# Kernel tuning notes

Measured on AMD Instinct MI355X. Metric: run time of the kernel, lower is better.

The kernel has to match this reference:

```python
import jax, jax.numpy as jnp
import numpy as np

N_NODES = 50000
N_EDGES = 800000
D_IN = 256
D_OUT = 256


def setup_inputs() -> dict:
    key = jax.random.key(0)
    ks = jax.random.split(key, 8)
    x = jax.random.normal(ks[0], (N_NODES, D_IN), dtype=jnp.float32)
    edge_index = jax.random.randint(ks[1], (2, N_EDGES), 0, N_NODES, dtype=jnp.int64)
    W_src = jax.random.normal(ks[2], (D_IN, D_OUT), dtype=jnp.float32) * 0.05
    b_src = jax.random.normal(ks[3], (D_OUT,), dtype=jnp.float32) * 0.05
    W_dst = jax.random.normal(ks[4], (D_IN, D_OUT), dtype=jnp.float32) * 0.05
    b_dst = jax.random.normal(ks[5], (D_OUT,), dtype=jnp.float32) * 0.05
    W_self = jax.random.normal(ks[6], (D_IN, D_OUT), dtype=jnp.float32) * 0.05
    b_self = jax.random.normal(ks[7], (D_OUT,), dtype=jnp.float32) * 0.05
    return {"x": x, "edge_index": edge_index, "W_src": W_src, "b_src": b_src,
            "W_dst": W_dst, "b_dst": b_dst, "W_self": W_self, "b_self": b_self}


def reference(x, edge_index, W_src, b_src, W_dst, b_dst, W_self, b_self):
    # LEConv: messages = src_linear(x[row]) - dst_linear(x[col]);
    # scatter-add messages into destination nodes (col); add self_linear(x).
    # Linear commutes with row-gather, so project once on [N, d] then gather.
    row, col = edge_index[0], edge_index[1]
    src = x @ W_src + b_src            # [N, D_OUT]
    dst = x @ W_dst + b_dst            # [N, D_OUT]
    messages = src[row] - dst[col]     # [E, D_OUT]
    agg = jax.ops.segment_sum(messages, col, num_segments=x.shape[0])  # [N, D_OUT]
    return x @ W_self + b_self + agg
```

## Files before the change

### kernel.cpp

```cpp
#include <hip/hip_runtime.h>

#define D 256

typedef unsigned short ushort_t;
typedef unsigned int uint_t;
typedef __attribute__((ext_vector_type(8))) short short8;
typedef __attribute__((ext_vector_type(4))) float floatx4;

static __device__ __forceinline__ ushort_t f2bf(float f) {
    union { float f; uint_t u; } c; c.f = f;
    uint_t r = (c.u + 0x7FFFu + ((c.u >> 16) & 1u)) >> 16;
    return (ushort_t)r;
}
static __device__ __forceinline__ float bf2f(ushort_t b) {
    union { uint_t u; float f; } c; c.u = ((uint_t)b) << 16;
    return c.f;
}

static __device__ __forceinline__ void async16(const void* g, void* l) {
    __builtin_amdgcn_global_load_lds(
        (const __attribute__((address_space(1))) void*)g,
        (__attribute__((address_space(3))) void*)l, 16, 0, 0);
}

__global__ void prep_kernel(const int* __restrict__ col, int* __restrict__ deg,
                            int* __restrict__ rank,
                            const float* __restrict__ x, ushort_t* __restrict__ xh,
                            const float* __restrict__ Wself, const float* __restrict__ Wsrc,
                            const float* __restrict__ Wdst, ushort_t* __restrict__ BT,
                            int E, int total8, int degB, int cvtB) {
    int b = blockIdx.x;
    if (b < degB) {
        int e = b * 256 + threadIdx.x;
        if (e < E) rank[e] = atomicAdd(&deg[col[e]], 1);
    } else if (b < degB + cvtB) {
        int i = (b - degB) * 256 + threadIdx.x;
        if (i >= total8) return;
        float4 a = ((const float4*)x)[i * 2];
        float4 bb = ((const float4*)x)[i * 2 + 1];
        uint4 o;
        o.x = f2bf(a.x) | ((uint_t)f2bf(a.y) << 16);
        o.y = f2bf(a.z) | ((uint_t)f2bf(a.w) << 16);
        o.z = f2bf(bb.x) | ((uint_t)f2bf(bb.y) << 16);
        o.w = f2bf(bb.z) | ((uint_t)f2bf(bb.w) << 16);
        ((uint4*)xh)[i] = o;
    } else {
        int id = (b - degB - cvtB) * 256 + threadIdx.x;
        if (id >= 256 * 768) return;
        int j = id / 768, k = id % 768;
        float v;
        if (k < 256)      v = Wself[(size_t)k * 256 + j];
        else if (k < 512) v = Wsrc [(size_t)(k - 256) * 256 + j];
        else              v = Wdst [(size_t)(k - 512) * 256 + j];
        BT[id] = f2bf(v);
    }
}

__global__ __launch_bounds__(256) void scanA(const int* __restrict__ deg,
                                             int* __restrict__ off,
                                             int* __restrict__ partials, int n4) {
    __shared__ int wtot[4];
    const int tid = threadIdx.x, lane = tid & 63, wid = tid >> 6;
    int i4 = blockIdx.x * 256 + tid;
    int4 v = (i4 < n4) ? ((const int4*)deg)[i4] : make_int4(0, 0, 0, 0);
    int s = v.x + v.y + v.z + v.w;
    int incl = s;
    #pragma unroll
    for (int st = 1; st < 64; st <<= 1) {
        int t = __shfl_up(incl, st, 64);
        if (lane >= st) incl += t;
    }
    if (lane == 63) wtot[wid] = incl;
    __syncthreads();
    int wbase = 0;
    #pragma unroll
    for (int w = 0; w < 4; ++w) if (w < wid) wbase += wtot[w];
    int excl = incl - s + wbase;
    if (i4 < n4) {
        int4 o;
        o.x = excl; o.y = o.x + v.x; o.z = o.y + v.y; o.w = o.z + v.z;
        ((int4*)off)[i4] = o;
    }
    if (tid == 0) partials[blockIdx.x] = wtot[0] + wtot[1] + wtot[2] + wtot[3];
}

__global__ __launch_bounds__(256) void scanC(int* __restrict__ off,
                                             const int* __restrict__ partials, int n4) {
    __shared__ int base_s;
    const int tid = threadIdx.x;
    if (tid < 64) {
        int v = (tid < blockIdx.x) ? partials[tid] : 0;
        #pragma unroll
        for (int st = 32; st; st >>= 1) v += __shfl_down(v, st, 64);
        if (tid == 0) base_s = v;
    }
    __syncthreads();
    int base = base_s;
    int i4 = blockIdx.x * 256 + tid;
    if (i4 < n4) {
        int4 o = ((int4*)off)[i4];
        o.x += base; o.y += base; o.z += base; o.w += base;
        ((int4*)off)[i4] = o;
    }
}

__global__ void fill_kernel(const int* __restrict__ row, const int* __restrict__ col,
                            const int* __restrict__ rank, const int* __restrict__ off,
                            int* __restrict__ bucket, int E) {
    int e = blockIdx.x * blockDim.x + threadIdx.x;
    if (e >= E) return;
    bucket[off[col[e]] + rank[e]] = row[e];
}

__global__ __launch_bounds__(256) void segsum_kernel(const ushort_t* __restrict__ xh,
                                                     const int* __restrict__ off,
                                                     const int* __restrict__ deg,
                                                     const int* __restrict__ bucket,
                                                     ushort_t* __restrict__ Gh, int N) {
    int node = blockIdx.x * 4 + (threadIdx.x >> 6);
    int lane = threadIdx.x & 63;
    if (node >= N) return;
    int start = off[node];
    int cnt = deg[node];
    float a0 = 0.f, a1 = 0.f, a2 = 0.f, a3 = 0.f;
    int i = 0;
    for (; i + 4 <= cnt; i += 4) {
        int r0 = bucket[start + i];
        int r1 = bucket[start + i + 1];
        int r2 = bucket[start + i + 2];
        int r3 = bucket[start + i + 3];
        ushort4 v0 = ((const ushort4*)(xh + (size_t)r0 * D))[lane];
        ushort4 v1 = ((const ushort4*)(xh + (size_t)r1 * D))[lane];
        ushort4 v2 = ((const ushort4*)(xh + (size_t)r2 * D))[lane];
        ushort4 v3 = ((const ushort4*)(xh + (size_t)r3 * D))[lane];
        a0 += (bf2f(v0.x) + bf2f(v1.x)) + (bf2f(v2.x) + bf2f(v3.x));
        a1 += (bf2f(v0.y) + bf2f(v1.y)) + (bf2f(v2.y) + bf2f(v3.y));
        a2 += (bf2f(v0.z) + bf2f(v1.z)) + (bf2f(v2.z) + bf2f(v3.z));
        a3 += (bf2f(v0.w) + bf2f(v1.w)) + (bf2f(v2.w) + bf2f(v3.w));
    }
    for (; i < cnt; ++i) {
        int r0 = bucket[start + i];
        ushort4 v0 = ((const ushort4*)(xh + (size_t)r0 * D))[lane];
        a0 += bf2f(v0.x); a1 += bf2f(v0.y); a2 += bf2f(v0.z); a3 += bf2f(v0.w);
    }
    ushort4 o;
    o.x = f2bf(a0); o.y = f2bf(a1); o.z = f2bf(a2); o.w = f2bf(a3);
    ((ushort4*)(Gh + (size_t)node * D))[lane] = o;
}

__global__ __launch_bounds__(256, 2) void mfma_gemm(
    const ushort_t* __restrict__ xh, const ushort_t* __restrict__ Gh,
    const ushort_t* __restrict__ BT, const int* __restrict__ deg,
    const float* __restrict__ bsrc, const float* __restrict__ bdst,
    const float* __restrict__ bself, float* __restrict__ out, int N)
{
    __shared__ ushort_t As[8][64][8];
    __shared__ ushort_t Bs[8][64][8];
    __shared__ ushort_t Ds[8][64][8];

    const int tid = threadIdx.x;
    const int lane = tid & 63, wave = tid >> 6;
    const int quad = lane >> 4, l15 = lane & 15;
    const int mg = (wave >> 1) * 4, ng = (wave & 1) * 4;
    const int mbase = blockIdx.x * 128, nbase = blockIdx.y * 128;

    const int ga0 = wave * 2, ga1 = ga0 + 1;
    int ar0 = mbase + ga0 * 16 + l15; if (ar0 >= N) ar0 = N - 1;
    int ar1 = mbase + ga1 * 16 + l15; if (ar1 >= N) ar1 = N - 1;
    const size_t aoff0 = (size_t)ar0 * 256 + quad * 8;
    const size_t aoff1 = (size_t)ar1 * 256 + quad * 8;
    const ushort_t* bp0 = BT + (size_t)(nbase + ga0 * 16 + l15) * 768 + quad * 8;
    const ushort_t* bp1 = BT + (size_t)(nbase + ga1 * 16 + l15) * 768 + quad * 8;

    floatx4 acc1[4][4] = {};
    floatx4 acc2[4][4] = {};

    for (int kt = 0; kt < 16; ++kt) {
        const ushort_t* Asrc = (kt < 8) ? xh : Gh;
        const int ka = (kt & 7) * 32;
        const int kb = kt * 32;
        async16(Asrc + aoff0 + ka, &As[ga0][0][0]);
        async16(Asrc + aoff1 + ka, &As[ga1][0][0]);
        async16(bp0 + kb, &Bs[ga0][0][0]);
        async16(bp1 + kb, &Bs[ga1][0][0]);
        if (kt < 8) {
            async16(bp0 + 512 + kb, &Ds[ga0][0][0]);
            async16(bp1 + 512 + kb, &Ds[ga1][0][0]);
        }
        __syncthreads();

        short8 af[4], bfr[4];
        #pragma unroll
        for (int im = 0; im < 4; ++im)
            af[im] = *(const short8*)(&As[mg + im][lane][0]);
        #pragma unroll
        for (int in = 0; in < 4; ++in)
            bfr[in] = *(const short8*)(&Bs[ng + in][lane][0]);
        #pragma unroll
        for (int im = 0; im < 4; ++im)
            #pragma unroll
            for (int in = 0; in < 4; ++in)
                acc1[im][in] = __builtin_amdgcn_mfma_f32_16x16x32_bf16(
                    af[im], bfr[in], acc1[im][in], 0, 0, 0);
        if (kt < 8) {
            short8 df[4];
            #pragma unroll
            for (int in = 0; in < 4; ++in)
                df[in] = *(const short8*)(&Ds[ng + in][lane][0]);
            #pragma unroll
            for (int im = 0; im < 4; ++im)
                #pragma unroll
                for (int in = 0; in < 4; ++in)
                    acc2[im][in] = __builtin_amdgcn_mfma_f32_16x16x32_bf16(
                        af[im], df[in], acc2[im][in], 0, 0, 0);
        }
        __syncthreads();
    }

    float degv[4][4];
    #pragma unroll
    for (int im = 0; im < 4; ++im)
        #pragma unroll
        for (int r = 0; r < 4; ++r) {
            int gm = mbase + (wave >> 1) * 64 + im * 16 + quad * 4 + r;
            degv[im][r] = (gm < N) ? (float)deg[gm] : 0.f;
        }

    #pragma unroll
    for (int in = 0; in < 4; ++in) {
        int gn = nbase + (wave & 1) * 64 + in * 16 + l15;
        float bs = bself[gn];
        float db = bsrc[gn] - bdst[gn];
        #pragma unroll
        for (int im = 0; im < 4; ++im) {
            #pragma unroll
            for (int r = 0; r < 4; ++r) {
                int gm = mbase + (wave >> 1) * 64 + im * 16 + quad * 4 + r;
                if (gm < N) {
                    float d = degv[im][r];
                    out[(size_t)gm * 256 + gn] =
                        acc1[im][in][r] - d * acc2[im][in][r] + bs + d * db;
                }
            }
        }
    }
}

extern "C" void kernel_launch(void* const* d_in, const int* in_sizes, int n_in,
                              void* d_out, int out_size, void* d_ws, size_t ws_size,
                              hipStream_t stream) {
    const float* x     = (const float*)d_in[0];
    const int*   eidx  = (const int*)d_in[1];
    const float* Wsrc  = (const float*)d_in[2];
    const float* bsrc  = (const float*)d_in[3];
    const float* Wdst  = (const float*)d_in[4];
    const float* bdst  = (const float*)d_in[5];
    const float* Wself = (const float*)d_in[6];
    const float* bself = (const float*)d_in[7];
    float* out = (float*)d_out;

    const int N = in_sizes[0] / D;
    const int E = in_sizes[1] / 2;
    const int* row = eidx;
    const int* col = eidx + E;

    char* p = (char*)d_ws;
    ushort_t* xh  = (ushort_t*)p;        p += (size_t)N * D * sizeof(ushort_t);
    ushort_t* Gh  = (ushort_t*)p;        int* rank = (int*)p;
                                         p += (size_t)N * D * sizeof(ushort_t);
    ushort_t* BT  = (ushort_t*)p;        p += (size_t)768 * 256 * sizeof(ushort_t);
    int* deg      = (int*)p;             p += (size_t)N * sizeof(int);
    int* off      = (int*)p;             p += (size_t)N * sizeof(int);
    int* partials = (int*)p;             p += 64 * sizeof(int);
    int* bucket   = (int*)p;

    hipMemsetAsync(deg, 0, (size_t)N * sizeof(int), stream);

    const int total8 = N * D / 8;
    const int degB = (E + 255) / 256;
    const int cvtB = (total8 + 255) / 256;
    const int btB  = (256 * 768 + 255) / 256;
    prep_kernel<<<degB + cvtB + btB, 256, 0, stream>>>(col, deg, rank, x, xh,
                                                       Wself, Wsrc, Wdst, BT,
                                                       E, total8, degB, cvtB);
    const int n4 = N / 4;
    const int nblk = (n4 + 255) / 256;
    scanA<<<nblk, 256, 0, stream>>>(deg, off, partials, n4);
    scanC<<<nblk, 256, 0, stream>>>(off, partials, n4);
    fill_kernel<<<(E + 255) / 256, 256, 0, stream>>>(row, col, rank, off, bucket, E);
    segsum_kernel<<<(N + 3) / 4, 256, 0, stream>>>(xh, off, deg, bucket, Gh, N);

    dim3 grid((N + 127) / 128, 2);
    mfma_gemm<<<grid, 256, 0, stream>>>(xh, Gh, BT, deg, bsrc, bdst, bself, out, N);
}
```

Measured before the change: 276.5 us.

## Double-buffer LDS tiles in MFMA GEMM to overlap global loads with compute

After: 314.8 us. +13.8%, slower.

```diff
diff --git a/kernel.cpp b/kernel.cpp
--- a/kernel.cpp
+++ b/kernel.cpp
@@ -148,15 +148,15 @@
     ((ushort4*)(Gh + (size_t)node * D))[lane] = o;
 }
 
-__global__ __launch_bounds__(256, 2) void mfma_gemm(
+__global__ __launch_bounds__(256, 3) void mfma_gemm(
     const ushort_t* __restrict__ xh, const ushort_t* __restrict__ Gh,
     const ushort_t* __restrict__ BT, const int* __restrict__ deg,
     const float* __restrict__ bsrc, const float* __restrict__ bdst,
     const float* __restrict__ bself, float* __restrict__ out, int N)
 {
-    __shared__ ushort_t As[8][64][8];
-    __shared__ ushort_t Bs[8][64][8];
-    __shared__ ushort_t Ds[8][64][8];
+    __shared__ ushort_t As[2][8][64][8];
+    __shared__ ushort_t Bs[2][8][64][8];
+    __shared__ ushort_t Ds[2][8][64][8];
 
     const int tid = threadIdx.x;
     const int lane = tid & 63, wave = tid >> 6;
@@ -175,27 +175,41 @@
     floatx4 acc1[4][4] = {};
     floatx4 acc2[4][4] = {};
 
+    async16(xh + aoff0, &As[0][ga0][0][0]);
+    async16(xh + aoff1, &As[0][ga1][0][0]);
+    async16(bp0, &Bs[0][ga0][0][0]);
+    async16(bp1, &Bs[0][ga1][0][0]);
+    async16(bp0 + 512, &Ds[0][ga0][0][0]);
+    async16(bp1 + 512, &Ds[0][ga1][0][0]);
+    asm volatile("s_waitcnt vmcnt(0)" ::: "memory");
+    __builtin_amdgcn_s_barrier();
+
+    #pragma unroll
     for (int kt = 0; kt < 16; ++kt) {
-        const ushort_t* Asrc = (kt < 8) ? xh : Gh;
-        const int ka = (kt & 7) * 32;
-        const int kb = kt * 32;
-        async16(Asrc + aoff0 + ka, &As[ga0][0][0]);
-        async16(Asrc + aoff1 + ka, &As[ga1][0][0]);
-        async16(bp0 + kb, &Bs[ga0][0][0]);
-        async16(bp1 + kb, &Bs[ga1][0][0]);
-        if (kt < 8) {
-            async16(bp0 + 512 + kb, &Ds[ga0][0][0]);
-            async16(bp1 + 512 + kb, &Ds[ga1][0][0]);
-        }
-        __syncthreads();
+        const int cur = kt & 1, nxt = cur ^ 1;
+
+        if (kt < 15) {
+            const int k1 = kt + 1;
+            const ushort_t* Asrc = (k1 < 8) ? xh : Gh;
+            const int ka = (k1 & 7) * 32;
+            const int kb = k1 * 32;
+            async16(Asrc + aoff0 + ka, &As[nxt][ga0][0][0]);
+            async16(Asrc + aoff1 + ka, &As[nxt][ga1][0][0]);
+            async16(bp0 + kb, &Bs[nxt][ga0][0][0]);
+            async16(bp1 + kb, &Bs[nxt][ga1][0][0]);
+            if (k1 < 8) {
+                async16(bp0 + 512 + kb, &Ds[nxt][ga0][0][0]);
+                async16(bp1 + 512 + kb, &Ds[nxt][ga1][0][0]);
+            }
+        }
 
         short8 af[4], bfr[4];
         #pragma unroll
         for (int im = 0; im < 4; ++im)
-            af[im] = *(const short8*)(&As[mg + im][lane][0]);
+            af[im] = *(const short8*)(&As[cur][mg + im][lane][0]);
         #pragma unroll
         for (int in = 0; in < 4; ++in)
-            bfr[in] = *(const short8*)(&Bs[ng + in][lane][0]);
+            bfr[in] = *(const short8*)(&Bs[cur][ng + in][lane][0]);
         #pragma unroll
         for (int im = 0; im < 4; ++im)
             #pragma unroll
@@ -206,7 +220,7 @@
             short8 df[4];
             #pragma unroll
             for (int in = 0; in < 4; ++in)
-                df[in] = *(const short8*)(&Ds[ng + in][lane][0]);
+                df[in] = *(const short8*)(&Ds[cur][ng + in][lane][0]);
             #pragma unroll
             for (int im = 0; im < 4; ++im)
                 #pragma unroll
@@ -214,7 +228,11 @@
                     acc2[im][in] = __builtin_amdgcn_mfma_f32_16x16x32_bf16(
                         af[im], df[in], acc2[im][in], 0, 0, 0);
         }
-        __syncthreads();
+
+        if (kt < 15) {
+            asm volatile("s_waitcnt vmcnt(0)" ::: "memory");
+            __builtin_amdgcn_s_barrier();
+        }
     }
 
     float degv[4][4];
```

## Triple-buffer LDS tiles in MFMA GEMM with vmcnt-based async prefetch

Applied to the files above, without the earlier changes.

Measured after the change: 284.3 us. 1.03x slower.

```diff
diff --git a/kernel.cpp b/kernel.cpp
--- a/kernel.cpp
+++ b/kernel.cpp
@@ -21,6 +21,16 @@
     __builtin_amdgcn_global_load_lds(
         (const __attribute__((address_space(1))) void*)g,
         (__attribute__((address_space(3))) void*)l, 16, 0, 0);
+}
+
+static __device__ __forceinline__ void wait_vmcnt_rt(int n) {
+    switch (n) {
+        case 0:  asm volatile("s_waitcnt vmcnt(0)"  ::: "memory"); break;
+        case 4:  asm volatile("s_waitcnt vmcnt(4)"  ::: "memory"); break;
+        case 8:  asm volatile("s_waitcnt vmcnt(8)"  ::: "memory"); break;
+        case 10: asm volatile("s_waitcnt vmcnt(10)" ::: "memory"); break;
+        default: asm volatile("s_waitcnt vmcnt(12)" ::: "memory"); break;
+    }
 }
 
 __global__ void prep_kernel(const int* __restrict__ col, int* __restrict__ deg,
@@ -154,9 +164,9 @@
     const float* __restrict__ bsrc, const float* __restrict__ bdst,
     const float* __restrict__ bself, float* __restrict__ out, int N)
 {
-    __shared__ ushort_t As[8][64][8];
-    __shared__ ushort_t Bs[8][64][8];
-    __shared__ ushort_t Ds[8][64][8];
+    __shared__ ushort_t As[3][8][64][8];
+    __shared__ ushort_t Bs[3][8][64][8];
+    __shared__ ushort_t Ds[3][8][64][8];
 
     const int tid = threadIdx.x;
     const int lane = tid & 63, wave = tid >> 6;
@@ -175,27 +185,41 @@
     floatx4 acc1[4][4] = {};
     floatx4 acc2[4][4] = {};
 
+    auto stage = [&](int s, int b) {
+        const ushort_t* Ap = (s < 8) ? xh : Gh;
+        const int ka = (s & 7) * 32;
+        const int kb = s * 32;
+        async16(Ap + aoff0 + ka, &As[b][ga0][0][0]);
+        async16(Ap + aoff1 + ka, &As[b][ga1][0][0]);
+        async16(bp0 + kb, &Bs[b][ga0][0][0]);
+        async16(bp1 + kb, &Bs[b][ga1][0][0]);
+        if (s < 8) {
+            async16(bp0 + 512 + kb, &Ds[b][ga0][0][0]);
+            async16(bp1 + 512 + kb, &Ds[b][ga1][0][0]);
+        }
+    };
+
+    stage(0, 0);
+    stage(1, 1);
+
+    #pragma unroll
     for (int kt = 0; kt < 16; ++kt) {
-        const ushort_t* Asrc = (kt < 8) ? xh : Gh;
-        const int ka = (kt & 7) * 32;
-        const int kb = kt * 32;
-        async16(Asrc + aoff0 + ka, &As[ga0][0][0]);
-        async16(Asrc + aoff1 + ka, &As[ga1][0][0]);
-        async16(bp0 + kb, &Bs[ga0][0][0]);
-        async16(bp1 + kb, &Bs[ga1][0][0]);
-        if (kt < 8) {
-            async16(bp0 + 512 + kb, &Ds[ga0][0][0]);
-            async16(bp1 + 512 + kb, &Ds[ga1][0][0]);
-        }
-        __syncthreads();
+        const int cur = kt % 3;
+
+        if (kt < 14) stage(kt + 2, (kt + 2) % 3);
+
+        const int l1 = (kt + 1 < 8) ? 6 : ((kt + 1 < 16) ? 4 : 0);
+        const int l2 = (kt + 2 < 8) ? 6 : ((kt + 2 < 16) ? 4 : 0);
+        wait_vmcnt_rt(l1 + l2);
+        __builtin_amdgcn_s_barrier();
 
         short8 af[4], bfr[4];
         #pragma unroll
         for (int im = 0; im < 4; ++im)
-            af[im] = *(const short8*)(&As[mg + im][lane][0]);
+            af[im] = *(const short8*)(&As[cur][mg + im][lane][0]);
         #pragma unroll
         for (int in = 0; in < 4; ++in)
-            bfr[in] = *(const short8*)(&Bs[ng + in][lane][0]);
+            bfr[in] = *(const short8*)(&Bs[cur][ng + in][lane][0]);
         #pragma unroll
         for (int im = 0; im < 4; ++im)
             #pragma unroll
@@ -206,7 +230,7 @@
             short8 df[4];
             #pragma unroll
             for (int in = 0; in < 4; ++in)
-                df[in] = *(const short8*)(&Ds[ng + in][lane][0]);
+                df[in] = *(const short8*)(&Ds[cur][ng + in][lane][0]);
             #pragma unroll
             for (int im = 0; im < 4; ++im)
                 #pragma unroll
@@ -214,7 +238,8 @@
                     acc2[im][in] = __builtin_amdgcn_mfma_f32_16x16x32_bf16(
                         af[im], df[in], acc2[im][in], 0, 0, 0);
         }
-        __syncthreads();
+
+        if (kt < 15) __builtin_amdgcn_s_barrier();
     }
 
     float degv[4][4];
```

## Use 16-byte gathers with half-wave edge split and persistent grid in segsum

Applied to the files above, without the earlier changes.

Result: slower. 302.6 us (+9.4%).

```diff
diff --git a/kernel.cpp b/kernel.cpp
--- a/kernel.cpp
+++ b/kernel.cpp
@@ -116,36 +116,53 @@
                                                      const int* __restrict__ off,
                                                      const int* __restrict__ deg,
                                                      const int* __restrict__ bucket,
-                                                     ushort_t* __restrict__ Gh, int N) {
-    int node = blockIdx.x * 4 + (threadIdx.x >> 6);
-    int lane = threadIdx.x & 63;
-    if (node >= N) return;
-    int start = off[node];
-    int cnt = deg[node];
-    float a0 = 0.f, a1 = 0.f, a2 = 0.f, a3 = 0.f;
-    int i = 0;
-    for (; i + 4 <= cnt; i += 4) {
-        int r0 = bucket[start + i];
-        int r1 = bucket[start + i + 1];
-        int r2 = bucket[start + i + 2];
-        int r3 = bucket[start + i + 3];
-        ushort4 v0 = ((const ushort4*)(xh + (size_t)r0 * D))[lane];
-        ushort4 v1 = ((const ushort4*)(xh + (size_t)r1 * D))[lane];
-        ushort4 v2 = ((const ushort4*)(xh + (size_t)r2 * D))[lane];
-        ushort4 v3 = ((const ushort4*)(xh + (size_t)r3 * D))[lane];
-        a0 += (bf2f(v0.x) + bf2f(v1.x)) + (bf2f(v2.x) + bf2f(v3.x));
-        a1 += (bf2f(v0.y) + bf2f(v1.y)) + (bf2f(v2.y) + bf2f(v3.y));
-        a2 += (bf2f(v0.z) + bf2f(v1.z)) + (bf2f(v2.z) + bf2f(v3.z));
-        a3 += (bf2f(v0.w) + bf2f(v1.w)) + (bf2f(v2.w) + bf2f(v3.w));
-    }
-    for (; i < cnt; ++i) {
-        int r0 = bucket[start + i];
-        ushort4 v0 = ((const ushort4*)(xh + (size_t)r0 * D))[lane];
-        a0 += bf2f(v0.x); a1 += bf2f(v0.y); a2 += bf2f(v0.z); a3 += bf2f(v0.w);
-    }
-    ushort4 o;
-    o.x = f2bf(a0); o.y = f2bf(a1); o.z = f2bf(a2); o.w = f2bf(a3);
-    ((ushort4*)(Gh + (size_t)node * D))[lane] = o;
+                                                     ushort_t* __restrict__ Gh,
+                                                     int N, int nwaves) {
+    const int gwid = blockIdx.x * 4 + (threadIdx.x >> 6);
+    const int lane = threadIdx.x & 63;
+    const int half = lane >> 5;
+    const size_t eoff = (size_t)(lane & 31) * 8;
+
+    for (int node = gwid; node < N; node += nwaves) {
+        const int start = off[node];
+        const int cnt = deg[node];
+        float a[8] = {0.f, 0.f, 0.f, 0.f, 0.f, 0.f, 0.f, 0.f};
+        int i = 0;
+        for (; i + 8 <= cnt; i += 8) {
+            int r0 = bucket[start + i + 0 + half];
+            int r1 = bucket[start + i + 2 + half];
+            int r2 = bucket[start + i + 4 + half];
+            int r3 = bucket[start + i + 6 + half];
+            short8 v0 = *(const short8*)(xh + (size_t)r0 * D + eoff);
+            short8 v1 = *(const short8*)(xh + (size_t)r1 * D + eoff);
+            short8 v2 = *(const short8*)(xh + (size_t)r2 * D + eoff);
+            short8 v3 = *(const short8*)(xh + (size_t)r3 * D + eoff);
+            #pragma unroll
+            for (int j = 0; j < 8; ++j)
+                a[j] += (bf2f((ushort_t)v0[j]) + bf2f((ushort_t)v1[j])) +
+                        (bf2f((ushort_t)v2[j]) + bf2f((ushort_t)v3[j]));
+        }
+        for (; i + 2 <= cnt; i += 2) {
+            int r = bucket[start + i + half];
+            short8 v = *(const short8*)(xh + (size_t)r * D + eoff);
+            #pragma unroll
+            for (int j = 0; j < 8; ++j) a[j] += bf2f((ushort_t)v[j]);
+        }
+        if (i < cnt && half == 0) {
+            int r = bucket[start + i];
+            short8 v = *(const short8*)(xh + (size_t)r * D + eoff);
+            #pragma unroll
+            for (int j = 0; j < 8; ++j) a[j] += bf2f((ushort_t)v[j]);
+        }
+        #pragma unroll
+        for (int j = 0; j < 8; ++j) a[j] += __shfl_xor(a[j], 32, 64);
+        if (half == 0) {
+            short8 o;
+            #pragma unroll
+            for (int j = 0; j < 8; ++j) o[j] = (short)f2bf(a[j]);
+            *(short8*)(Gh + (size_t)node * D + eoff) = o;
+        }
+    }
 }
 
 __global__ __launch_bounds__(256, 2) void mfma_gemm(
@@ -288,7 +305,10 @@
     scanA<<<nblk, 256, 0, stream>>>(deg, off, partials, n4);
     scanC<<<nblk, 256, 0, stream>>>(off, partials, n4);
     fill_kernel<<<(E + 255) / 256, 256, 0, stream>>>(row, col, rank, off, bucket, E);
-    segsum_kernel<<<(N + 3) / 4, 256, 0, stream>>>(xh, off, deg, bucket, Gh, N);
+
+    const int sblocks = 512;
+    segsum_kernel<<<sblocks, 256, 0, stream>>>(xh, off, deg, bucket, Gh, N,
+                                               sblocks * 4);
 
     dim3 grid((N + 127) / 128, 2);
     mfma_gemm<<<grid, 256, 0, stream>>>(xh, Gh, BT, deg, bsrc, bdst, bself, out, N);
```
